# Performance work log

Measured on AMD Instinct MI355X. Metric: run time of the kernel, lower is better.

Reference implementation:

```python
import jax, jax.numpy as jnp
import numpy as np

# Dimensions derived from init_kwargs
NODE_NUMBER = 4096
IN_FEATURES = 2
N_KERNELS = 1
S = NODE_NUMBER * IN_FEATURES            # input_size = 8192
OUT = S * N_KERNELS                      # output size = 8192
NNZ = 524288                             # number of (row, col, weight_pos) triples
WNUM = 30000                             # shared weight pool size
BNUM = 100                               # shared bias pool size


def setup_inputs() -> dict:
    key = jax.random.key(0)
    ks = jax.random.split(key, 7)
    bound = 1.0 / np.sqrt(WNUM)  # init scale as in the torch module
    return {
        "x": jax.random.normal(ks[0], (S,), dtype=jnp.float32),
        "Param_W": (jax.random.normal(ks[1], (WNUM,), dtype=jnp.float32) * bound).astype(jnp.float32),
        "Param_b": (jax.random.normal(ks[2], (BNUM,), dtype=jnp.float32) * bound).astype(jnp.float32),
        "rows": jax.random.randint(ks[3], (NNZ,), 0, S, dtype=jnp.int32),
        "cols": jax.random.randint(ks[4], (NNZ,), 0, OUT, dtype=jnp.int32),
        "wpos": jax.random.randint(ks[5], (NNZ,), 0, WNUM, dtype=jnp.int32),
        "bias_pos": jax.random.randint(ks[6], (OUT,), 0, BNUM, dtype=jnp.int32),
    }


def reference(x, Param_W, Param_b, rows, cols, wpos, bias_pos):
    # Gather shared scalar parameters into the dense per-graph weight matrix
    # W[row, col] = Param_W[weight_pos]  (precomputed label-based index map)
    W = jnp.zeros((S, OUT), dtype=x.dtype).at[rows, cols].set(Param_W[wpos])
    # Gather per-position bias from shared bias pool (indexed by node label)
    b = Param_b[bias_pos]
    # Convolution-like matmul: flattened node features times gathered matrix
    return x @ W + b
```

## Files before the change

### kernel.cpp

```cpp
#include <hip/hip_runtime.h>

#define NNZ_  524288
#define S_    8192
#define OUT_  8192
#define CAP   192

__global__ void __launch_bounds__(256) scatter_kernel(
    const int* __restrict__ cols, int* __restrict__ cnt, int* __restrict__ buckets) {
    int i = blockIdx.x * blockDim.x + threadIdx.x;
    if (i >= NNZ_) return;
    int c = cols[i];
    int p = atomicAdd(&cnt[c], 1);
    if (p < CAP) buckets[c * CAP + p] = i;
}

__global__ void __launch_bounds__(256) col_kernel(
    const float* __restrict__ x, const float* __restrict__ W,
    const float* __restrict__ b, const int* __restrict__ rows,
    const int* __restrict__ wpos, const int* __restrict__ bias_pos,
    const int* __restrict__ cnt, const int* __restrict__ buckets,
    float* __restrict__ out) {
    __shared__ int srow[4][CAP];
    __shared__ int sidx[4][CAP];
    const int wave = threadIdx.x >> 6;
    const int lane = threadIdx.x & 63;
    const int c = blockIdx.x * 4 + wave;

    int k = cnt[c];
    if (k > CAP) k = CAP;

    for (int m = lane; m < k; m += 64) {
        int i = buckets[c * CAP + m];
        sidx[wave][m] = i;
        srow[wave][m] = rows[i];
    }
    __syncthreads();

    float acc = 0.f;
    for (int m = lane; m < k; m += 64) {
        int i = sidx[wave][m];
        int r = srow[wave][m];
        bool win = true;
        for (int t = 0; t < k; ++t) {
            if (srow[wave][t] == r && sidx[wave][t] > i) { win = false; break; }
        }
        if (win) acc += x[r] * W[wpos[i]];
    }

    for (int off = 32; off; off >>= 1) acc += __shfl_down(acc, off, 64);
    if (lane == 0) out[c] = acc + b[bias_pos[c]];
}

extern "C" void kernel_launch(void* const* d_in, const int* in_sizes, int n_in,
                              void* d_out, int out_size, void* d_ws, size_t ws_size,
                              hipStream_t stream) {
    const float* x    = (const float*)d_in[0];
    const float* Pw   = (const float*)d_in[1];
    const float* Pb   = (const float*)d_in[2];
    const int*   rows = (const int*)d_in[3];
    const int*   cols = (const int*)d_in[4];
    const int*   wpos = (const int*)d_in[5];
    const int*   bpos = (const int*)d_in[6];
    float*       out  = (float*)d_out;

    int* cnt     = (int*)d_ws;
    int* buckets = cnt + OUT_;

    hipMemsetAsync(cnt, 0, OUT_ * sizeof(int), stream);
    scatter_kernel<<<NNZ_ / 256, 256, 0, stream>>>(cols, cnt, buckets);
    col_kernel<<<OUT_ / 4, 256, 0, stream>>>(x, Pw, Pb, rows, wpos, bpos, cnt, buckets, out);
}
```

Before: 138.3 us.

## Fuse memset, scatter and column reduce into one cooperative kernel

Replaces the memset plus two kernel launches with a single cooperative kernel that zeroes counts, buckets entries, and reduces columns, separated by grid-wide syncs. Bucket entries now pack the row index and the NNZ index into one 32-bit word, so the duplicate check reads one shared array and the separate rows gather in the reduce phase goes away. The goal is to cut launch overhead and the per-entry rows load. In exchange it adds grid sync cost and the limits of a persistent grid of 1024 blocks, and the packing assumes rows fit in 13 bits and indices in 19 bits.

```diff
diff --git a/kernel.cpp b/kernel.cpp
--- a/kernel.cpp
+++ b/kernel.cpp
@@ -1,54 +1,65 @@
 #include <hip/hip_runtime.h>
+#include <hip/hip_cooperative_groups.h>
+
+namespace cg = cooperative_groups;
 
 #define NNZ_  524288
 #define S_    8192
 #define OUT_  8192
 #define CAP   192
+#define GRID  1024
+#define BLK   256
 
-__global__ void __launch_bounds__(256) scatter_kernel(
-    const int* __restrict__ cols, int* __restrict__ cnt, int* __restrict__ buckets) {
-    int i = blockIdx.x * blockDim.x + threadIdx.x;
-    if (i >= NNZ_) return;
-    int c = cols[i];
-    int p = atomicAdd(&cnt[c], 1);
-    if (p < CAP) buckets[c * CAP + p] = i;
-}
-
-__global__ void __launch_bounds__(256) col_kernel(
+__global__ void __launch_bounds__(BLK, 4) fused_kernel(
     const float* __restrict__ x, const float* __restrict__ W,
     const float* __restrict__ b, const int* __restrict__ rows,
-    const int* __restrict__ wpos, const int* __restrict__ bias_pos,
-    const int* __restrict__ cnt, const int* __restrict__ buckets,
-    float* __restrict__ out) {
-    __shared__ int srow[4][CAP];
-    __shared__ int sidx[4][CAP];
+    const int* __restrict__ cols, const int* __restrict__ wpos,
+    const int* __restrict__ bias_pos,
+    int* __restrict__ cnt, unsigned* __restrict__ buckets,
+    float* __restrict__ out)
+{
+    cg::grid_group grid = cg::this_grid();
+    const int tid   = blockIdx.x * BLK + threadIdx.x;
+    const int total = GRID * BLK;
+
+    for (int c = tid; c < OUT_; c += total) cnt[c] = 0;
+    grid.sync();
+
+    for (int i = tid; i < NNZ_; i += total) {
+        int c = cols[i];
+        unsigned e = ((unsigned)rows[i] << 19) | (unsigned)i;
+        int p = atomicAdd(&cnt[c], 1);
+        if (p < CAP) buckets[c * CAP + p] = e;
+    }
+    grid.sync();
+
+    __shared__ unsigned sb[BLK / 64][CAP];
     const int wave = threadIdx.x >> 6;
     const int lane = threadIdx.x & 63;
-    const int c = blockIdx.x * 4 + wave;
+    const int gw   = tid >> 6;
+    const int nw   = total >> 6;
 
-    int k = cnt[c];
-    if (k > CAP) k = CAP;
-
-    for (int m = lane; m < k; m += 64) {
-        int i = buckets[c * CAP + m];
-        sidx[wave][m] = i;
-        srow[wave][m] = rows[i];
+    unsigned* s = sb[wave];
+    for (int c = gw; c < OUT_; c += nw) {
+        int k = cnt[c]; if (k > CAP) k = CAP;
+        for (int m = lane; m < k; m += 64) s[m] = buckets[c * CAP + m];
+        float acc = 0.f;
+        for (int m = lane; m < k; m += 64) {
+            unsigned mine = s[m];
+            bool win = true;
+            for (int t = 0; t < k; ++t) {
+                unsigned o = s[t];
+                if (((mine ^ o) >> 19) == 0u && o > mine) { win = false; break; }
+            }
+            if (win) {
+                int i = (int)(mine & 0x7FFFFu);
+                int r = (int)(mine >> 19);
+                acc += x[r] * W[wpos[i]];
+            }
+        }
+        for (int off = 32; off; off >>= 1) acc += __shfl_down(acc, off, 64);
+        if (lane == 0) out[c] = acc + b[bias_pos[c]];
     }
-    __syncthreads();
-
-    float acc = 0.f;
-    for (int m = lane; m < k; m += 64) {
-        int i = sidx[wave][m];
-        int r = srow[wave][m];
-        bool win = true;
-        for (int t = 0; t < k; ++t) {
-            if (srow[wave][t] == r && sidx[wave][t] > i) { win = false; break; }
-        }
-        if (win) acc += x[r] * W[wpos[i]];
-    }
-
-    for (int off = 32; off; off >>= 1) acc += __shfl_down(acc, off, 64);
-    if (lane == 0) out[c] = acc + b[bias_pos[c]];
 }
 
 extern "C" void kernel_launch(void* const* d_in, const int* in_sizes, int n_in,
@@ -63,10 +74,12 @@
     const int*   bpos = (const int*)d_in[6];
     float*       out  = (float*)d_out;
 
-    int* cnt     = (int*)d_ws;
-    int* buckets = cnt + OUT_;
+    int*      cnt     = (int*)d_ws;
+    unsigned* buckets = (unsigned*)(cnt + OUT_);
 
-    hipMemsetAsync(cnt, 0, OUT_ * sizeof(int), stream);
-    scatter_kernel<<<NNZ_ / 256, 256, 0, stream>>>(cols, cnt, buckets);
-    col_kernel<<<OUT_ / 4, 256, 0, stream>>>(x, Pw, Pb, rows, wpos, bpos, cnt, buckets, out);
+    void* args[] = { (void*)&x, (void*)&Pw, (void*)&Pb, (void*)&rows,
+                     (void*)&cols, (void*)&wpos, (void*)&bpos,
+                     (void*)&cnt, (void*)&buckets, (void*)&out };
+    hipLaunchCooperativeKernel((const void*)fused_kernel, dim3(GRID), dim3(BLK),
+                               args, 0, stream);
 }
```

After: 319.4 us. +131.0%, slower.

## Pack row and entry index into bucket words and vectorize scatter

Applied to the files above, without the earlier changes.

The scatter kernel now reads cols and rows as int4, handles four entries per thread, and stores a packed word (row<<19 | entry index) in each bucket. The column kernel reads the packed words directly, so it no longer gathers rows[i] randomly and uses a single shared array for the duplicate-detection scan. The block-wide barrier is removed because each wave only touches its own slice. This relies on NNZ fitting in 19 bits and rows in 13 bits, and on intra-wave LDS ordering without an explicit barrier.

```diff
diff --git a/kernel.cpp b/kernel.cpp
--- a/kernel.cpp
+++ b/kernel.cpp
@@ -6,47 +6,48 @@
 #define CAP   192
 
 __global__ void __launch_bounds__(256) scatter_kernel(
-    const int* __restrict__ cols, int* __restrict__ cnt, int* __restrict__ buckets) {
-    int i = blockIdx.x * blockDim.x + threadIdx.x;
-    if (i >= NNZ_) return;
-    int c = cols[i];
-    int p = atomicAdd(&cnt[c], 1);
-    if (p < CAP) buckets[c * CAP + p] = i;
+    const int* __restrict__ rows, const int* __restrict__ cols,
+    int* __restrict__ cnt, unsigned* __restrict__ buckets)
+{
+    const int t = blockIdx.x * 256 + threadIdx.x;
+    const int4 c = ((const int4*)cols)[t];
+    const int4 r = ((const int4*)rows)[t];
+    const int base = t * 4;
+    const int p0 = atomicAdd(&cnt[c.x], 1);
+    const int p1 = atomicAdd(&cnt[c.y], 1);
+    const int p2 = atomicAdd(&cnt[c.z], 1);
+    const int p3 = atomicAdd(&cnt[c.w], 1);
+    if (p0 < CAP) buckets[c.x * CAP + p0] = ((unsigned)r.x << 19) | (unsigned)(base + 0);
+    if (p1 < CAP) buckets[c.y * CAP + p1] = ((unsigned)r.y << 19) | (unsigned)(base + 1);
+    if (p2 < CAP) buckets[c.z * CAP + p2] = ((unsigned)r.z << 19) | (unsigned)(base + 2);
+    if (p3 < CAP) buckets[c.w * CAP + p3] = ((unsigned)r.w << 19) | (unsigned)(base + 3);
 }
 
 __global__ void __launch_bounds__(256) col_kernel(
     const float* __restrict__ x, const float* __restrict__ W,
-    const float* __restrict__ b, const int* __restrict__ rows,
-    const int* __restrict__ wpos, const int* __restrict__ bias_pos,
-    const int* __restrict__ cnt, const int* __restrict__ buckets,
-    float* __restrict__ out) {
-    __shared__ int srow[4][CAP];
-    __shared__ int sidx[4][CAP];
+    const float* __restrict__ b, const int* __restrict__ wpos,
+    const int* __restrict__ bias_pos, const int* __restrict__ cnt,
+    const unsigned* __restrict__ buckets, float* __restrict__ out)
+{
+    __shared__ unsigned sb[4][CAP];
     const int wave = threadIdx.x >> 6;
     const int lane = threadIdx.x & 63;
     const int c = blockIdx.x * 4 + wave;
 
-    int k = cnt[c];
-    if (k > CAP) k = CAP;
-
-    for (int m = lane; m < k; m += 64) {
-        int i = buckets[c * CAP + m];
-        sidx[wave][m] = i;
-        srow[wave][m] = rows[i];
-    }
-    __syncthreads();
+    int k = cnt[c]; if (k > CAP) k = CAP;
+    unsigned* s = sb[wave];
+    for (int m = lane; m < k; m += 64) s[m] = buckets[c * CAP + m];
 
     float acc = 0.f;
     for (int m = lane; m < k; m += 64) {
-        int i = sidx[wave][m];
-        int r = srow[wave][m];
+        const unsigned mine = s[m];
         bool win = true;
-        for (int t = 0; t < k; ++t) {
-            if (srow[wave][t] == r && sidx[wave][t] > i) { win = false; break; }
+        for (int tt = 0; tt < k; ++tt) {
+            const unsigned o = s[tt];
+            if (((mine ^ o) >> 19) == 0u && o > mine) { win = false; break; }
         }
-        if (win) acc += x[r] * W[wpos[i]];
+        if (win) acc += x[mine >> 19] * W[wpos[mine & 0x7FFFFu]];
     }
-
     for (int off = 32; off; off >>= 1) acc += __shfl_down(acc, off, 64);
     if (lane == 0) out[c] = acc + b[bias_pos[c]];
 }
@@ -63,10 +64,10 @@
     const int*   bpos = (const int*)d_in[6];
     float*       out  = (float*)d_out;
 
-    int* cnt     = (int*)d_ws;
-    int* buckets = cnt + OUT_;
+    int*      cnt     = (int*)d_ws;
+    unsigned* buckets = (unsigned*)(cnt + OUT_);
 
     hipMemsetAsync(cnt, 0, OUT_ * sizeof(int), stream);
-    scatter_kernel<<<NNZ_ / 256, 256, 0, stream>>>(cols, cnt, buckets);
-    col_kernel<<<OUT_ / 4, 256, 0, stream>>>(x, Pw, Pb, rows, wpos, bpos, cnt, buckets, out);
+    scatter_kernel<<<NNZ_ / 4 / 256, 256, 0, stream>>>(rows, cols, cnt, buckets);
+    col_kernel<<<OUT_ / 4, 256, 0, stream>>>(x, Pw, Pb, wpos, bpos, cnt, buckets, out);
 }
```

Result: faster. 124.1 us (-10.3%).
